# Optimization experiments

Hardware: AMD Instinct MI355X
Metric: run time of the kernel (lower is better)

Reference implementation:

```python
import jax, jax.numpy as jnp
import numpy as np

N_E = 16384      # codebook size
E_DIM = 32       # codebook vector dim (== channel dim of z)
BETA = 0.25      # commitment loss weight
ENT_RATIO = 0.1  # entropy loss ratio
TEMP = 0.01      # entropy loss temperature


def _l2norm(x, eps=1e-12):
    # matches F.normalize(p=2, dim=-1): x / max(||x||, eps)
    n = jnp.sqrt(jnp.sum(x * x, axis=-1, keepdims=True))
    return x / jnp.maximum(n, eps)


def _entropy_loss(affinity):
    # affinity: (T, N_E)
    fa = affinity / TEMP
    probs = jax.nn.softmax(fa, axis=-1)
    log_probs = jax.nn.log_softmax(fa + 1e-05, axis=-1)
    avg_probs = jnp.mean(probs, axis=0)
    avg_entropy = -jnp.sum(avg_probs * jnp.log(avg_probs + 1e-05))
    sample_entropy = -jnp.mean(jnp.sum(probs * log_probs, axis=-1))
    return sample_entropy - avg_entropy


def setup_inputs() -> dict:
    key = jax.random.key(0)
    k1, k2 = jax.random.split(key)
    z = jax.random.normal(k1, (32, E_DIM, 16, 16), dtype=jnp.float32)
    # torch init: uniform(-1/n_e, 1/n_e) then l2-normalized rows
    emb = jax.random.uniform(k2, (N_E, E_DIM), dtype=jnp.float32,
                             minval=-1.0 / N_E, maxval=1.0 / N_E)
    emb = _l2norm(emb)
    return {"z": z, "embedding": emb}


def reference(z, embedding):
    # z: (b, c, h, w) -> (b, h, w, c)
    zb = jnp.transpose(z, (0, 2, 3, 1))
    zb = _l2norm(zb)                       # l2_norm=True path
    zf = zb.reshape(-1, E_DIM)             # (T, d), T = b*h*w
    emb = _l2norm(embedding)               # (N_E, d)
    # squared L2 distances (cdist expansion)
    d = (jnp.sum(zf * zf, axis=1, keepdims=True)
         + jnp.sum(emb * emb, axis=1)
         - 2.0 * jnp.einsum('td,nd->tn', zf, emb))   # (T, N_E)
    idx = jnp.argmin(d, axis=1)            # (T,)
    z_q = emb[idx].reshape(zb.shape)       # (b, h, w, c)
    # training losses
    vq_loss = jnp.mean((z_q - jax.lax.stop_gradient(zb)) ** 2)
    commit_loss = BETA * jnp.mean((jax.lax.stop_gradient(z_q) - zb) ** 2)
    entropy_loss = ENT_RATIO * _entropy_loss(-d)
    # straight-through estimator
    z_q_st = zb + jax.lax.stop_gradient(z_q - zb)
    out = jnp.transpose(z_q_st, (0, 3, 1, 2))  # back to (b, c, h, w)
    return out, vq_loss, commit_loss, entropy_loss
```

## Files before the change

### kernel.cpp

```cpp
#include <hip/hip_runtime.h>


#define N_E 16384
#define ED 32
#define T 8192
#define NS1 16
#define SKIPM -36.0f
#define PHT 8

#define K2 288.53900817779268f
#define NS2F -144.26950408889634f
#define BIAS1 -208.53900817779268f
#define LN2 0.6931471805599453f

typedef __attribute__((ext_vector_type(8))) short s16x8;
typedef __attribute__((ext_vector_type(4))) float f32x4;

__device__ __forceinline__ float fexp2(float x) { return __builtin_amdgcn_exp2f(x); }
__device__ __forceinline__ float flog2(float x) { return __builtin_amdgcn_logf(x); }
__device__ __forceinline__ float fmed3(float a, float b, float c) {
  return __builtin_amdgcn_fmed3f(a, b, c);
}

__device__ __forceinline__ float midband(float key) {
  return __uint_as_float((__float_as_uint(key) & 0xFFFFFC00u) | 512u);
}

__device__ __forceinline__ void gload16(const void* g, void* l) {
  __builtin_amdgcn_global_load_lds(
      (const __attribute__((address_space(1))) void*)g,
      (__attribute__((address_space(3))) void*)l, 16, 0, 0);
}

__device__ __forceinline__ unsigned short f2bf(float x) {
  unsigned u = __float_as_uint(x);
  unsigned r = (u + 0x7FFFu + ((u >> 16) & 1u)) >> 16;
  return (unsigned short)r;
}
__device__ __forceinline__ float bf2f(unsigned short h) {
  return __uint_as_float(((unsigned)h) << 16);
}

__device__ __forceinline__ float dot32x(const float* __restrict__ p,
    float4 z0, float4 z1, float4 z2, float4 z3,
    float4 z4, float4 z5, float4 z6, float4 z7) {
  const float4* e = (const float4*)p;
  float a0 = 0.f, a1 = 0.f, a2 = 0.f, a3 = 0.f; float4 q;
  q = e[0]; a0 = fmaf(q.x, z0.x, a0); a0 = fmaf(q.y, z0.y, a0);
            a0 = fmaf(q.z, z0.z, a0); a0 = fmaf(q.w, z0.w, a0);
  q = e[1]; a1 = fmaf(q.x, z1.x, a1); a1 = fmaf(q.y, z1.y, a1);
            a1 = fmaf(q.z, z1.z, a1); a1 = fmaf(q.w, z1.w, a1);
  q = e[2]; a2 = fmaf(q.x, z2.x, a2); a2 = fmaf(q.y, z2.y, a2);
            a2 = fmaf(q.z, z2.z, a2); a2 = fmaf(q.w, z2.w, a2);
  q = e[3]; a3 = fmaf(q.x, z3.x, a3); a3 = fmaf(q.y, z3.y, a3);
            a3 = fmaf(q.z, z3.z, a3); a3 = fmaf(q.w, z3.w, a3);
  q = e[4]; a0 = fmaf(q.x, z4.x, a0); a0 = fmaf(q.y, z4.y, a0);
            a0 = fmaf(q.z, z4.z, a0); a0 = fmaf(q.w, z4.w, a0);
  q = e[5]; a1 = fmaf(q.x, z5.x, a1); a1 = fmaf(q.y, z5.y, a1);
            a1 = fmaf(q.z, z5.z, a1); a1 = fmaf(q.w, z5.w, a1);
  q = e[6]; a2 = fmaf(q.x, z6.x, a2); a2 = fmaf(q.y, z6.y, a2);
            a2 = fmaf(q.z, z6.z, a2); a2 = fmaf(q.w, z6.w, a2);
  q = e[7]; a3 = fmaf(q.x, z7.x, a3); a3 = fmaf(q.y, z7.y, a3);
            a3 = fmaf(q.z, z7.z, a3); a3 = fmaf(q.w, z7.w, a3);
  return (a0 + a1) + (a2 + a3);
}

__device__ __forceinline__ void split_store_t(short* __restrict__ base,
    int row, int g, float4 va, float4 vb, float sc) {
  float f[8] = { va.x * sc, va.y * sc, va.z * sc, va.w * sc,
                 vb.x * sc, vb.y * sc, vb.z * sc, vb.w * sc };
  s16x8 H, L;
#pragma unroll
  for (int e = 0; e < 8; ++e) {
    unsigned short h = f2bf(f[e]);
    H[e] = (short)h;
    L[e] = (short)f2bf(f[e] - bf2f(h));
  }
  s16x8* p = (s16x8*)base;
  const int tile = row >> 4, c = row & 15;
  p[tile * 128 + g * 16 + c] = H;
  p[tile * 128 + 64 + g * 16 + c] = L;
}

__global__ __launch_bounds__(256) void k_prep(const float* __restrict__ emb,
    const float* __restrict__ z, float* __restrict__ embn,
    float* __restrict__ ses2, float* __restrict__ zf, float* __restrict__ a02,
    short* __restrict__ ehl, short* __restrict__ zhl, float* __restrict__ avg,
    float* __restrict__ scal) {
  if (blockIdx.x < 64) {
    int n = blockIdx.x * 256 + threadIdx.x;
    const float4* r4 = (const float4*)(emb + (size_t)n * ED);
    float4 v[8]; float s = 0.f;
#pragma unroll
    for (int j = 0; j < 8; ++j) {
      v[j] = r4[j];
      s = fmaf(v[j].x, v[j].x, s); s = fmaf(v[j].y, v[j].y, s);
      s = fmaf(v[j].z, v[j].z, s); s = fmaf(v[j].w, v[j].w, s);
    }
    float inv = 1.0f / fmaxf(sqrtf(s), 1e-12f);
    float s2 = 0.f;
    float4* o4 = (float4*)(embn + (size_t)n * ED);
#pragma unroll
    for (int j = 0; j < 8; ++j) {
      float4 w; w.x = v[j].x * inv; w.y = v[j].y * inv;
      w.z = v[j].z * inv; w.w = v[j].w * inv;
      o4[j] = w; v[j] = w;
      s2 = fmaf(w.x, w.x, s2); s2 = fmaf(w.y, w.y, s2);
      s2 = fmaf(w.z, w.z, s2); s2 = fmaf(w.w, w.w, s2);
    }
    ses2[n] = NS2F * s2;
#pragma unroll
    for (int g = 0; g < 4; ++g)
      split_store_t(ehl, n, g, v[2 * g], v[2 * g + 1], 1.0f);
  } else if (blockIdx.x < 96) {
    int t = (blockIdx.x - 64) * 256 + threadIdx.x;
    int b = t >> 8, hw = t & 255;
    const float* base = z + (size_t)b * (ED * 256) + hw;
    float4 v[8]; float s = 0.f;
#pragma unroll
    for (int j = 0; j < 8; ++j) {
      float4 w;
      w.x = base[(4 * j + 0) * 256]; w.y = base[(4 * j + 1) * 256];
      w.z = base[(4 * j + 2) * 256]; w.w = base[(4 * j + 3) * 256];
      v[j] = w;
      s = fmaf(w.x, w.x, s); s = fmaf(w.y, w.y, s);
      s = fmaf(w.z, w.z, s); s = fmaf(w.w, w.w, s);
    }
    float inv = 1.0f / fmaxf(sqrtf(s), 1e-12f);
    float s2 = 0.f;
    float4* o4 = (float4*)(zf + (size_t)t * ED);
#pragma unroll
    for (int j = 0; j < 8; ++j) {
      float4 w; w.x = v[j].x * inv; w.y = v[j].y * inv;
      w.z = v[j].z * inv; w.w = v[j].w * inv;
      o4[j] = w; v[j] = w;
      s2 = fmaf(w.x, w.x, s2); s2 = fmaf(w.y, w.y, s2);
      s2 = fmaf(w.z, w.z, s2); s2 = fmaf(w.w, w.w, s2);
    }
    a02[t] = NS2F * s2;
#pragma unroll
    for (int g = 0; g < 4; ++g)
      split_store_t(zhl, t, g, v[2 * g], v[2 * g + 1], K2);
  } else if (blockIdx.x < 160) {
    avg[(blockIdx.x - 96) * 256 + threadIdx.x] = 0.f;
  } else {
    if (threadIdx.x < 4) scal[threadIdx.x] = 0.f;
  }
}

__global__ __launch_bounds__(256, 4) void k_pass1(
    const short* __restrict__ ehl, const short* __restrict__ zhl,
    float* __restrict__ cand1, float* __restrict__ cand2) {
  const int tid = threadIdx.x;
  const int lane = tid & 63, wv = tid >> 6;
  const int q = lane >> 4, c = lane & 15;
  const int rowbase = blockIdx.x * 128 + wv * 32;
  const int NT = (N_E / NS1) / 16;
  const int NP = NT / PHT;

  __shared__ s16x8 dbuf[2][PHT * 128];

  const s16x8* zg = (const s16x8*)zhl;
  const int atile = rowbase >> 4;
  s16x8 ah[2], al[2];
#pragma unroll
  for (int rg = 0; rg < 2; ++rg) {
    ah[rg] = zg[(atile + rg) * 128 + lane];
    al[rg] = zg[(atile + rg) * 128 + 64 + lane];
  }

  f32x4 bias;
#pragma unroll
  for (int r = 0; r < 4; ++r) bias[r] = BIAS1;

  float m1[2][4], m2[2][4];
#pragma unroll
  for (int rg = 0; rg < 2; ++rg)
#pragma unroll
    for (int k = 0; k < 4; ++k) { m1[rg][k] = -1e30f; m2[rg][k] = -1e30f; }

  const s16x8* eg = (const s16x8*)ehl + (size_t)(blockIdx.y * ((N_E / NS1) >> 4)) * 128;

#pragma unroll
  for (int j = 0; j < 4; ++j)
    gload16(eg + wv * 256 + j * 64 + lane, &dbuf[0][wv * 256 + j * 64]);
  __syncthreads();

  for (int p = 0; p < NP; ++p) {
    if (p + 1 < NP) {
      const s16x8* gs = eg + (p + 1) * (PHT * 128);
      s16x8* lb = &dbuf[(p + 1) & 1][0];
#pragma unroll
      for (int j = 0; j < 4; ++j)
        gload16(gs + wv * 256 + j * 64 + lane, lb + wv * 256 + j * 64);
    }
    const s16x8* bb = &dbuf[p & 1][0];
#pragma unroll
    for (int tt = 0; tt < PHT; ++tt) {
      s16x8 bh = bb[tt * 128 + lane], bl = bb[tt * 128 + 64 + lane];
      const unsigned tuc = (((unsigned)(p * PHT + tt)) << 4) | (unsigned)c;
#pragma unroll
      for (int rg = 0; rg < 2; ++rg) {
        f32x4 acc = __builtin_amdgcn_mfma_f32_16x16x32_bf16(ah[rg], bh, bias, 0, 0, 0);
        acc = __builtin_amdgcn_mfma_f32_16x16x32_bf16(al[rg], bh, acc, 0, 0, 0);
        acc = __builtin_amdgcn_mfma_f32_16x16x32_bf16(ah[rg], bl, acc, 0, 0, 0);
#pragma unroll
        for (int r = 0; r < 4; ++r) {
          float key = __uint_as_float((__float_as_uint(acc[r]) & 0xFFFFFC00u) | tuc);
          m2[rg][r] = fmed3(key, m1[rg][r], m2[rg][r]);
          m1[rg][r] = fmaxf(m1[rg][r], key);
        }
      }
    }
    __syncthreads();
  }

  const int s = blockIdx.y;
#pragma unroll
  for (int rg = 0; rg < 2; ++rg) {
    float4 v1 = make_float4(m1[rg][0], m1[rg][1], m1[rg][2], m1[rg][3]);
    float4 v2 = make_float4(m2[rg][0], m2[rg][1], m2[rg][2], m2[rg][3]);
    const size_t base = (size_t)(s * 16 + c) * T + (rowbase + rg * 16 + q * 4);
    *(float4*)(cand1 + base) = v1;
    *(float4*)(cand2 + base) = v2;
  }
}

__global__ __launch_bounds__(256) void k_fin(
    const float* __restrict__ cand1, const float* __restrict__ cand2,
    const float* __restrict__ zf, const float* __restrict__ embn,
    const float* __restrict__ ses2, const float* __restrict__ a02,
    float* __restrict__ avg, float* __restrict__ scal,
    float* __restrict__ out) {
  const int tid = threadIdx.x;
  const int rr = tid & 15;
  const int g  = tid >> 4;
  const int row = blockIdx.x * 16 + rr;

  __shared__ float sZ[256], sS2[256], sk1[256], sk2[256];
  __shared__ int su1[256], su2[256];
  __shared__ float slZ[16], rsE[16], rvq[16];

  float ka[16], kb[16];
  float k1 = -1e30f, k2 = -1e30f; int u1 = 0, u2 = 0;
  float Z = 0.f, S2 = 0.f;
#pragma unroll
  for (int k = 0; k < 16; ++k) {
    const int u = g * 16 + k;
    const float ca = cand1[(size_t)u * T + row];
    const float cb = cand2[(size_t)u * T + row];
    ka[k] = ca; kb[k] = cb;
    if (ca > k1) { k2 = k1; u2 = u1; k1 = ca; u1 = u; }
    else if (ca > k2) { k2 = ca; u2 = u; }
    if (cb > k1) { k2 = k1; u2 = u1; k1 = cb; u1 = u; }
    else if (cb > k2) { k2 = cb; u2 = u; }
    const float fa = midband(ca), fb = midband(cb);
    const float ea = fexp2(fa), eb = fexp2(fb);
    Z += ea + eb;
    S2 = fmaf(ea, fa, S2); S2 = fmaf(eb, fb, S2);
  }
  sZ[tid] = Z; sS2[tid] = S2;
  sk1[tid] = k1; sk2[tid] = k2; su1[tid] = u1; su2[tid] = u2;
  __syncthreads();
  for (int st = 8; st >= 1; st >>= 1) {
    if (g < st) {
      const int o = tid + st * 16;
      sZ[tid] += sZ[o]; sS2[tid] += sS2[o];
      const float ok1 = sk1[o], ok2 = sk2[o];
      const int ou1 = su1[o], ou2 = su2[o];
      const float a1 = sk1[tid], a2 = sk2[tid];
      const int b1 = su1[tid];
      if (a1 >= ok1) {
        if (a2 < ok1) { sk2[tid] = ok1; su2[tid] = ou1; }
      } else {
        sk1[tid] = ok1; su1[tid] = ou1;
        if (ok2 >= a1) { sk2[tid] = ok2; su2[tid] = ou2; }
        else           { sk2[tid] = a1;  su2[tid] = b1; }
      }
    }
    __syncthreads();
  }
  if (g == 0) slZ[rr] = flog2(sZ[rr]);
  __syncthreads();
  const float lZ = slZ[rr];

#pragma unroll
  for (int k = 0; k < 16; ++k) {
    const int u = g * 16 + k;
    {
      const float dl = midband(ka[k]) - lZ;
      if (dl > SKIPM) {
        const unsigned kid = __float_as_uint(ka[k]) & 1023u;
        atomicAdd(&avg[(u >> 4) * 1024 + (int)((kid >> 4) << 4) + (int)(kid & 15u)],
                  fexp2(dl));
      }
    }
    {
      const float dl = midband(kb[k]) - lZ;
      if (dl > SKIPM) {
        const unsigned kid = __float_as_uint(kb[k]) & 1023u;
        atomicAdd(&avg[(u >> 4) * 1024 + (int)((kid >> 4) << 4) + (int)(kid & 15u)],
                  fexp2(dl));
      }
    }
  }

  if (g == 0) {
    rsE[rr] = sS2[rr] / sZ[rr] - lZ;
    const unsigned kk1 = __float_as_uint(sk1[rr]) & 1023u;
    const unsigned kk2 = __float_as_uint(sk2[rr]) & 1023u;
    const int i1 = (su1[rr] >> 4) * 1024 + (int)((kk1 >> 4) << 4) + (int)(kk1 & 15u);
    const int i2 = (su2[rr] >> 4) * 1024 + (int)((kk2 >> 4) << 4) + (int)(kk2 & 15u);
    const float a02t = a02[row];

    const float4* zr4 = (const float4*)(zf + (size_t)row * ED);
    float4 z0 = zr4[0], z1 = zr4[1], z2 = zr4[2], z3 = zr4[3];
    float4 z4 = zr4[4], z5 = zr4[5], z6 = zr4[6], z7 = zr4[7];
    float d1 = dot32x(embn + (size_t)i1 * ED, z0, z1, z2, z3, z4, z5, z6, z7);
    float d2 = dot32x(embn + (size_t)i2 * ED, z0, z1, z2, z3, z4, z5, z6, z7);
    float fb1 = fmaf(K2, d1, a02t + ses2[i1]);
    float fb2 = fmaf(K2, d2, a02t + ses2[i2]);
    int bi = (fb2 > fb1 || (fb2 == fb1 && i2 < i1)) ? i2 : i1;

    const int b = row >> 8, hw = row & 255;
    float* ob = out + (size_t)b * (ED * 256) + hw;
    float ss = 0.f;
    const float4* e4 = (const float4*)(embn + (size_t)bi * ED);
#pragma unroll
    for (int j = 0; j < 8; ++j) {
      float4 qv = e4[j];
      float4 zv = (j == 0) ? z0 : (j == 1) ? z1 : (j == 2) ? z2 : (j == 3) ? z3
                : (j == 4) ? z4 : (j == 5) ? z5 : (j == 6) ? z6 : z7;
      float df;
      df = qv.x - zv.x; ss = fmaf(df, df, ss); ob[(4 * j + 0) * 256] = zv.x + (qv.x - zv.x);
      df = qv.y - zv.y; ss = fmaf(df, df, ss); ob[(4 * j + 1) * 256] = zv.y + (qv.y - zv.y);
      df = qv.z - zv.z; ss = fmaf(df, df, ss); ob[(4 * j + 2) * 256] = zv.z + (qv.z - zv.z);
      df = qv.w - zv.w; ss = fmaf(df, df, ss); ob[(4 * j + 3) * 256] = zv.w + (qv.w - zv.w);
    }
    rvq[rr] = ss;
  }
  __syncthreads();
  if (tid == 0) {
    float se = 0.f, vq = 0.f;
    for (int i = 0; i < 16; ++i) { se += rsE[i]; vq += rvq[i]; }
    atomicAdd(&scal[0], se);
    atomicAdd(&scal[1], vq);
  }
}

__global__ __launch_bounds__(256) void k_last(const float* __restrict__ avg,
    const float* __restrict__ scal, float* __restrict__ out) {
  const int tid = threadIdx.x;
  __shared__ float red[256];
  float s = 0.f;
  for (int i = tid; i < N_E; i += 256) {
    float a = avg[i] * (1.0f / T);
    s += a * (flog2(a + 1e-5f) * LN2);
  }
  red[tid] = s;
  __syncthreads();
  for (int st = 128; st > 0; st >>= 1) {
    if (tid < st) red[tid] += red[tid + st];
    __syncthreads();
  }
  if (tid == 0) {
    float avg_entropy = -red[0];
    float sample_entropy = -(scal[0] * LN2) * (1.0f / T);
    float vq = scal[1] * (1.0f / (T * ED));
    out[T * ED + 0] = vq;
    out[T * ED + 1] = 0.25f * vq;
    out[T * ED + 2] = 0.1f * (sample_entropy - avg_entropy);
  }
}

extern "C" void kernel_launch(void* const* d_in, const int* in_sizes, int n_in,
                              void* d_out, int out_size, void* d_ws, size_t ws_size,
                              hipStream_t stream) {
  const float* z = (const float*)d_in[0];
  const float* emb = (const float*)d_in[1];
  float* out = (float*)d_out;
  float* w = (float*)d_ws;

  float* embn = w;
  float* ses2 = embn + 524288;
  float* zf   = ses2 + 16384;
  float* a02  = zf + 262144;
  short* ehl  = (short*)(a02 + 8192);
  short* zhl  = ehl + 1048576;
  float* cand1 = (float*)(zhl + 524288);
  float* cand2 = cand1 + 256 * T;
  float* avg  = cand2 + 256 * T;
  float* scal = avg + 16384;

  k_prep<<<161, 256, 0, stream>>>(emb, z, embn, ses2, zf, a02, ehl, zhl,
                                  avg, scal);
  k_pass1<<<dim3(T / 128, NS1), 256, 0, stream>>>(ehl, zhl, cand1, cand2);
  k_fin<<<T / 16, 256, 0, stream>>>(cand1, cand2, zf, embn, ses2, a02,
                                    avg, scal, out);
  k_last<<<1, 256, 0, stream>>>(avg, scal, out);
}
```

Before: 145.6 us.

## Drop codebook low-bf16 split, skip non-improving tiles, widen exact rescoring

Stores the codebook as a single bf16 half instead of a hi/lo pair, which cuts pass-1 MFMAs from three to two per tile and halves the codebook tile traffic. It also doubles tiles per LDS phase. Pass 1 now skips the top-2 update when no lane's score beats its running second-best minus a margin. The finalize kernel replaces the merge of the top-2 per row with an fp32 rescoring of every candidate within a threshold of the max, resolved by a packed 64-bit atomicMax. The lower codebook precision is meant to be covered by the wider rescoring window, at the cost of extra dot products and atomics, and it risks misranking near-ties if the threshold is too tight.

```diff
diff --git a/kernel.cpp b/kernel.cpp
--- a/kernel.cpp
+++ b/kernel.cpp
@@ -6,7 +6,8 @@
 #define T 8192
 #define NS1 16
 #define SKIPM -36.0f
-#define PHT 8
+#define SKP1M 0.0625f
+#define PHT 16
 
 #define K2 288.53900817779268f
 #define NS2F -144.26950408889634f
@@ -39,30 +40,6 @@
 }
 __device__ __forceinline__ float bf2f(unsigned short h) {
   return __uint_as_float(((unsigned)h) << 16);
-}
-
-__device__ __forceinline__ float dot32x(const float* __restrict__ p,
-    float4 z0, float4 z1, float4 z2, float4 z3,
-    float4 z4, float4 z5, float4 z6, float4 z7) {
-  const float4* e = (const float4*)p;
-  float a0 = 0.f, a1 = 0.f, a2 = 0.f, a3 = 0.f; float4 q;
-  q = e[0]; a0 = fmaf(q.x, z0.x, a0); a0 = fmaf(q.y, z0.y, a0);
-            a0 = fmaf(q.z, z0.z, a0); a0 = fmaf(q.w, z0.w, a0);
-  q = e[1]; a1 = fmaf(q.x, z1.x, a1); a1 = fmaf(q.y, z1.y, a1);
-            a1 = fmaf(q.z, z1.z, a1); a1 = fmaf(q.w, z1.w, a1);
-  q = e[2]; a2 = fmaf(q.x, z2.x, a2); a2 = fmaf(q.y, z2.y, a2);
-            a2 = fmaf(q.z, z2.z, a2); a2 = fmaf(q.w, z2.w, a2);
-  q = e[3]; a3 = fmaf(q.x, z3.x, a3); a3 = fmaf(q.y, z3.y, a3);
-            a3 = fmaf(q.z, z3.z, a3); a3 = fmaf(q.w, z3.w, a3);
-  q = e[4]; a0 = fmaf(q.x, z4.x, a0); a0 = fmaf(q.y, z4.y, a0);
-            a0 = fmaf(q.z, z4.z, a0); a0 = fmaf(q.w, z4.w, a0);
-  q = e[5]; a1 = fmaf(q.x, z5.x, a1); a1 = fmaf(q.y, z5.y, a1);
-            a1 = fmaf(q.z, z5.z, a1); a1 = fmaf(q.w, z5.w, a1);
-  q = e[6]; a2 = fmaf(q.x, z6.x, a2); a2 = fmaf(q.y, z6.y, a2);
-            a2 = fmaf(q.z, z6.z, a2); a2 = fmaf(q.w, z6.w, a2);
-  q = e[7]; a3 = fmaf(q.x, z7.x, a3); a3 = fmaf(q.y, z7.y, a3);
-            a3 = fmaf(q.z, z7.z, a3); a3 = fmaf(q.w, z7.w, a3);
-  return (a0 + a1) + (a2 + a3);
 }
 
 __device__ __forceinline__ void split_store_t(short* __restrict__ base,
@@ -80,6 +57,15 @@
   const int tile = row >> 4, c = row & 15;
   p[tile * 128 + g * 16 + c] = H;
   p[tile * 128 + 64 + g * 16 + c] = L;
+}
+
+__device__ __forceinline__ void split_store_h(short* __restrict__ base,
+    int row, int g, float4 va, float4 vb) {
+  float f[8] = { va.x, va.y, va.z, va.w, vb.x, vb.y, vb.z, vb.w };
+  s16x8 H;
+#pragma unroll
+  for (int e = 0; e < 8; ++e) H[e] = (short)f2bf(f[e]);
+  ((s16x8*)base)[(row >> 4) * 64 + g * 16 + (row & 15)] = H;
 }
 
 __global__ __launch_bounds__(256) void k_prep(const float* __restrict__ emb,
@@ -111,7 +97,7 @@
     ses2[n] = NS2F * s2;
 #pragma unroll
     for (int g = 0; g < 4; ++g)
-      split_store_t(ehl, n, g, v[2 * g], v[2 * g + 1], 1.0f);
+      split_store_h(ehl, n, g, v[2 * g], v[2 * g + 1]);
   } else if (blockIdx.x < 96) {
     int t = (blockIdx.x - 64) * 256 + threadIdx.x;
     int b = t >> 8, hw = t & 255;
@@ -158,7 +144,7 @@
   const int NT = (N_E / NS1) / 16;
   const int NP = NT / PHT;
 
-  __shared__ s16x8 dbuf[2][PHT * 128];
+  __shared__ s16x8 dbuf[2][PHT * 64];
 
   const s16x8* zg = (const s16x8*)zhl;
   const int atile = rowbase >> 4;
@@ -178,8 +164,9 @@
   for (int rg = 0; rg < 2; ++rg)
 #pragma unroll
     for (int k = 0; k < 4; ++k) { m1[rg][k] = -1e30f; m2[rg][k] = -1e30f; }
-
-  const s16x8* eg = (const s16x8*)ehl + (size_t)(blockIdx.y * ((N_E / NS1) >> 4)) * 128;
+  float m2min = -1e30f;
+
+  const s16x8* eg = (const s16x8*)ehl + (size_t)blockIdx.y * (64 * 64);
 
 #pragma unroll
   for (int j = 0; j < 4; ++j)
@@ -188,7 +175,7 @@
 
   for (int p = 0; p < NP; ++p) {
     if (p + 1 < NP) {
-      const s16x8* gs = eg + (p + 1) * (PHT * 128);
+      const s16x8* gs = eg + (p + 1) * (PHT * 64);
       s16x8* lb = &dbuf[(p + 1) & 1][0];
 #pragma unroll
       for (int j = 0; j < 4; ++j)
@@ -197,19 +184,28 @@
     const s16x8* bb = &dbuf[p & 1][0];
 #pragma unroll
     for (int tt = 0; tt < PHT; ++tt) {
-      s16x8 bh = bb[tt * 128 + lane], bl = bb[tt * 128 + 64 + lane];
+      s16x8 bh = bb[tt * 64 + lane];
       const unsigned tuc = (((unsigned)(p * PHT + tt)) << 4) | (unsigned)c;
-#pragma unroll
-      for (int rg = 0; rg < 2; ++rg) {
-        f32x4 acc = __builtin_amdgcn_mfma_f32_16x16x32_bf16(ah[rg], bh, bias, 0, 0, 0);
-        acc = __builtin_amdgcn_mfma_f32_16x16x32_bf16(al[rg], bh, acc, 0, 0, 0);
-        acc = __builtin_amdgcn_mfma_f32_16x16x32_bf16(ah[rg], bl, acc, 0, 0, 0);
+
+      f32x4 acc0 = __builtin_amdgcn_mfma_f32_16x16x32_bf16(ah[0], bh, bias, 0, 0, 0);
+      acc0 = __builtin_amdgcn_mfma_f32_16x16x32_bf16(al[0], bh, acc0, 0, 0, 0);
+      f32x4 acc1 = __builtin_amdgcn_mfma_f32_16x16x32_bf16(ah[1], bh, bias, 0, 0, 0);
+      acc1 = __builtin_amdgcn_mfma_f32_16x16x32_bf16(al[1], bh, acc1, 0, 0, 0);
+
+      float mx = fmaxf(fmaxf(fmaxf(acc0[0], acc0[1]), fmaxf(acc0[2], acc0[3])),
+                       fmaxf(fmaxf(acc1[0], acc1[1]), fmaxf(acc1[2], acc1[3])));
+      if (__any(mx > m2min - SKP1M)) {
 #pragma unroll
         for (int r = 0; r < 4; ++r) {
-          float key = __uint_as_float((__float_as_uint(acc[r]) & 0xFFFFFC00u) | tuc);
-          m2[rg][r] = fmed3(key, m1[rg][r], m2[rg][r]);
-          m1[rg][r] = fmaxf(m1[rg][r], key);
+          float k0 = __uint_as_float((__float_as_uint(acc0[r]) & 0xFFFFFC00u) | tuc);
+          m2[0][r] = fmed3(k0, m1[0][r], m2[0][r]);
+          m1[0][r] = fmaxf(m1[0][r], k0);
+          float k1v = __uint_as_float((__float_as_uint(acc1[r]) & 0xFFFFFC00u) | tuc);
+          m2[1][r] = fmed3(k1v, m1[1][r], m2[1][r]);
+          m1[1][r] = fmaxf(m1[1][r], k1v);
         }
+        m2min = fminf(fminf(fminf(m2[0][0], m2[0][1]), fminf(m2[0][2], m2[0][3])),
+                      fminf(fminf(m2[1][0], m2[1][1]), fminf(m2[1][2], m2[1][3])));
       }
     }
     __syncthreads();
@@ -237,90 +233,78 @@
   const int g  = tid >> 4;
   const int row = blockIdx.x * 16 + rr;
 
-  __shared__ float sZ[256], sS2[256], sk1[256], sk2[256];
-  __shared__ int su1[256], su2[256];
-  __shared__ float slZ[16], rsE[16], rvq[16];
+  __shared__ float sZ[256], sS2[256], sk1[256];
+  __shared__ unsigned long long rbest[16];
+  __shared__ float slZ[16], sth[16], rsE[16], rvq[16];
+  if (tid < 16) rbest[tid] = 0ull;
 
   float ka[16], kb[16];
-  float k1 = -1e30f, k2 = -1e30f; int u1 = 0, u2 = 0;
-  float Z = 0.f, S2 = 0.f;
+  float k1 = -1e30f, Z = 0.f, S2 = 0.f;
 #pragma unroll
   for (int k = 0; k < 16; ++k) {
     const int u = g * 16 + k;
     const float ca = cand1[(size_t)u * T + row];
     const float cb = cand2[(size_t)u * T + row];
     ka[k] = ca; kb[k] = cb;
-    if (ca > k1) { k2 = k1; u2 = u1; k1 = ca; u1 = u; }
-    else if (ca > k2) { k2 = ca; u2 = u; }
-    if (cb > k1) { k2 = k1; u2 = u1; k1 = cb; u1 = u; }
-    else if (cb > k2) { k2 = cb; u2 = u; }
+    k1 = fmaxf(k1, ca);
     const float fa = midband(ca), fb = midband(cb);
     const float ea = fexp2(fa), eb = fexp2(fb);
     Z += ea + eb;
-    S2 = fmaf(ea, fa, S2); S2 = fmaf(eb, fb, S2);
-  }
-  sZ[tid] = Z; sS2[tid] = S2;
-  sk1[tid] = k1; sk2[tid] = k2; su1[tid] = u1; su2[tid] = u2;
+    S2 = fmaf(ea, fa, fmaf(eb, fb, S2));
+  }
+  sZ[tid] = Z; sS2[tid] = S2; sk1[tid] = k1;
   __syncthreads();
   for (int st = 8; st >= 1; st >>= 1) {
     if (g < st) {
       const int o = tid + st * 16;
       sZ[tid] += sZ[o]; sS2[tid] += sS2[o];
-      const float ok1 = sk1[o], ok2 = sk2[o];
-      const int ou1 = su1[o], ou2 = su2[o];
-      const float a1 = sk1[tid], a2 = sk2[tid];
-      const int b1 = su1[tid];
-      if (a1 >= ok1) {
-        if (a2 < ok1) { sk2[tid] = ok1; su2[tid] = ou1; }
-      } else {
-        sk1[tid] = ok1; su1[tid] = ou1;
-        if (ok2 >= a1) { sk2[tid] = ok2; su2[tid] = ou2; }
-        else           { sk2[tid] = a1;  su2[tid] = b1; }
-      }
+      sk1[tid] = fmaxf(sk1[tid], sk1[o]);
     }
     __syncthreads();
   }
-  if (g == 0) slZ[rr] = flog2(sZ[rr]);
-  __syncthreads();
-  const float lZ = slZ[rr];
+  if (g == 0) { slZ[rr] = flog2(sZ[rr]); sth[rr] = sk1[rr] - 2.5f; }
+  __syncthreads();
+  const float lZ = slZ[rr], thr = sth[rr];
+  const float a02t = a02[row];
 
 #pragma unroll
   for (int k = 0; k < 16; ++k) {
     const int u = g * 16 + k;
-    {
-      const float dl = midband(ka[k]) - lZ;
-      if (dl > SKIPM) {
-        const unsigned kid = __float_as_uint(ka[k]) & 1023u;
-        atomicAdd(&avg[(u >> 4) * 1024 + (int)((kid >> 4) << 4) + (int)(kid & 15u)],
-                  fexp2(dl));
+#pragma unroll
+    for (int h = 0; h < 2; ++h) {
+      const float key = h ? kb[k] : ka[k];
+      const unsigned kid = __float_as_uint(key) & 1023u;
+      const int idx = (u >> 4) * 1024 + (int)((kid >> 4) << 4) + (int)(kid & 15u);
+      const float dl = midband(key) - lZ;
+      if (dl > SKIPM) atomicAdd(&avg[idx], fexp2(dl));
+      if (key > thr) {
+        const float4* er = (const float4*)(embn + (size_t)idx * ED);
+        const float4* zr = (const float4*)(zf + (size_t)row * ED);
+        float d = 0.f;
+#pragma unroll
+        for (int j = 0; j < 8; ++j) {
+          float4 a = er[j], b = zr[j];
+          d = fmaf(a.x, b.x, d); d = fmaf(a.y, b.y, d);
+          d = fmaf(a.z, b.z, d); d = fmaf(a.w, b.w, d);
+        }
+        const float fbx = fmaf(K2, d, a02t + ses2[idx]);
+        const unsigned ub = __float_as_uint(fbx);
+        const unsigned ord = ub ^ (unsigned)(((int)ub >> 31) | 0x80000000);
+        const unsigned long long pk =
+            ((unsigned long long)ord << 14) | (unsigned long long)(16383 - idx);
+        atomicMax(&rbest[rr], pk);
       }
     }
-    {
-      const float dl = midband(kb[k]) - lZ;
-      if (dl > SKIPM) {
-        const unsigned kid = __float_as_uint(kb[k]) & 1023u;
-        atomicAdd(&avg[(u >> 4) * 1024 + (int)((kid >> 4) << 4) + (int)(kid & 15u)],
-                  fexp2(dl));
-      }
-    }
-  }
+  }
+  __syncthreads();
 
   if (g == 0) {
     rsE[rr] = sS2[rr] / sZ[rr] - lZ;
-    const unsigned kk1 = __float_as_uint(sk1[rr]) & 1023u;
-    const unsigned kk2 = __float_as_uint(sk2[rr]) & 1023u;
-    const int i1 = (su1[rr] >> 4) * 1024 + (int)((kk1 >> 4) << 4) + (int)(kk1 & 15u);
-    const int i2 = (su2[rr] >> 4) * 1024 + (int)((kk2 >> 4) << 4) + (int)(kk2 & 15u);
-    const float a02t = a02[row];
+    const int bi = 16383 - (int)(rbest[rr] & 16383ull);
 
     const float4* zr4 = (const float4*)(zf + (size_t)row * ED);
     float4 z0 = zr4[0], z1 = zr4[1], z2 = zr4[2], z3 = zr4[3];
     float4 z4 = zr4[4], z5 = zr4[5], z6 = zr4[6], z7 = zr4[7];
-    float d1 = dot32x(embn + (size_t)i1 * ED, z0, z1, z2, z3, z4, z5, z6, z7);
-    float d2 = dot32x(embn + (size_t)i2 * ED, z0, z1, z2, z3, z4, z5, z6, z7);
-    float fb1 = fmaf(K2, d1, a02t + ses2[i1]);
-    float fb2 = fmaf(K2, d2, a02t + ses2[i2]);
-    int bi = (fb2 > fb1 || (fb2 == fb1 && i2 < i1)) ? i2 : i1;
 
     const int b = row >> 8, hw = row & 255;
     float* ob = out + (size_t)b * (ED * 256) + hw;
@@ -386,7 +370,7 @@
   float* zf   = ses2 + 16384;
   float* a02  = zf + 262144;
   short* ehl  = (short*)(a02 + 8192);
-  short* zhl  = ehl + 1048576;
+  short* zhl  = ehl + 524288;
   float* cand1 = (float*)(zhl + 524288);
   float* cand2 = cand1 + 256 * T;
   float* avg  = cand2 + 256 * T;
```

New measurement: 152.4 us. +4.7%, slower.
